# Kernel tuning notes

Measured on AMD Instinct MI355X. Metric: run time of the kernel, lower is better.

## Reference

```python
import jax, jax.numpy as jnp
import numpy as np

N, M, D, C, H = 8192, 8192, 256, 128, 128
LAMBDA_IB = 0.01
EPS = 1e-8


def setup_inputs() -> dict:
    key = jax.random.key(0)
    ks = jax.random.split(key, 8)
    s = 0.05  # small init so exp(critic) stays bounded
    return {
        "x1": jax.random.normal(ks[0], (N, D), jnp.float32),
        "x2": jax.random.normal(ks[1], (M, D), jnp.float32),
        "Wc": (jax.random.normal(ks[2], (D, C), jnp.float32) * s),
        "bc": jnp.zeros((C,), jnp.float32),
        "W1": (jax.random.normal(ks[3], (2 * C, H), jnp.float32) * s),
        "b1": jnp.zeros((H,), jnp.float32),
        "W2": (jax.random.normal(ks[4], (H, H), jnp.float32) * s),
        "b2": jnp.zeros((H,), jnp.float32),
        "W3": (jax.random.normal(ks[5], (H, 1), jnp.float32) * s),
        "b3": jnp.zeros((1,), jnp.float32),
        "perm": jax.random.permutation(ks[6], M).astype(jnp.int32),
    }


def _critic(z, W1, b1, W2, b2, W3, b3):
    h = jax.nn.relu(z @ W1 + b1)
    h = jax.nn.relu(h @ W2 + b2)
    return h @ W3 + b3  # [n, 1]


def reference(x1, x2, Wc, bc, W1, b1, W2, b2, W3, b3, perm):
    # pairwise cosine distance via normalize + GEMM (no NxMxD intermediate)
    n1 = jnp.maximum(jnp.linalg.norm(x1, axis=-1, keepdims=True), EPS)
    n2 = jnp.maximum(jnp.linalg.norm(x2, axis=-1, keepdims=True), EPS)
    distances = 1.0 - (x1 / n1) @ (x2 / n2).T  # [N, M]

    # compressor (shared linear) -> MINE MI lower bound
    xc1 = x1 @ Wc + bc  # [N, C]
    xc2 = x2 @ Wc + bc  # [M, C]
    xy = jnp.concatenate([xc1, xc2], axis=-1)          # joint
    xy_s = jnp.concatenate([xc1, xc2[perm]], axis=-1)  # marginal (shuffled)
    t_xy = _critic(xy, W1, b1, W2, b2, W3, b3)
    t_sh = _critic(xy_s, W1, b1, W2, b2, W3, b3)
    mi = jnp.mean(t_xy) - (jnp.mean(jnp.exp(t_sh)) + jnp.log(jnp.float32(2.0)))
    return distances + LAMBDA_IB * mi
```

## Files before the change

kernel.cpp:

```cpp
#include <hip/hip_runtime.h>
#include <hip/hip_bf16.h>
#include <stdint.h>
#include <stddef.h>


typedef __attribute__((ext_vector_type(8))) short bf16x8;
typedef __attribute__((ext_vector_type(4))) float f32x4;

__device__ __forceinline__ float bf2f(unsigned short u) {
  union { unsigned int i; float f; } a; a.i = ((unsigned int)u) << 16; return a.f;
}
__device__ __forceinline__ unsigned short f2bf(float f) {
  union { float f; unsigned int i; } a; a.f = f;
  unsigned int r = a.i + 0x7fffu + ((a.i >> 16) & 1u);
  return (unsigned short)(r >> 16);
}

#define NROWS 8192
#define DDIM 256
#define CDIM 128
#define HDIM 128

__global__ __launch_bounds__(256) void k_prep_weights(
    const float* __restrict__ Wc, const float* __restrict__ bc,
    const float* __restrict__ W1, const float* __restrict__ b1,
    const float* __restrict__ W2, const float* __restrict__ b2,
    const float* __restrict__ W3, const float* __restrict__ b3,
    unsigned short* __restrict__ WcT, unsigned short* __restrict__ W1T,
    unsigned short* __restrict__ W2T, float* __restrict__ fsmall,
    float* __restrict__ accum) {
  int t = blockIdx.x * 256 + threadIdx.x;
  int T = gridDim.x * 256;
  for (int i = t; i < DDIM * CDIM; i += T) {
    int k = i >> 7, n = i & 127;
    WcT[n * DDIM + k] = f2bf(Wc[i]);
    W1T[n * DDIM + k] = f2bf(W1[i]);
  }
  for (int i = t; i < HDIM * HDIM; i += T) {
    int k = i >> 7, n = i & 127;
    W2T[n * HDIM + k] = f2bf(W2[i]);
  }
  if (blockIdx.x == 0) {
    int tt = threadIdx.x;
    if (tt < 128) {
      fsmall[tt]       = bc[tt];
      fsmall[128 + tt] = b1[tt];
      fsmall[256 + tt] = b2[tt];
      fsmall[384 + tt] = W3[tt];
    }
    if (tt == 0) {
      fsmall[512] = b3[0];
      accum[0] = 0.0f; accum[1] = 0.0f;
    }
  }
}

__global__ __launch_bounds__(256) void k_prep_rows(
    const float* __restrict__ x1, const float* __restrict__ x2,
    unsigned short* __restrict__ xall,
    float* __restrict__ inva, float* __restrict__ invb) {
  int gtid = blockIdx.x * 256 + threadIdx.x;
  int wv = gtid >> 6;
  int lane = threadIdx.x & 63;
  int first = (wv < NROWS);
  const float* src = first ? x1 : x2;
  float* invp = first ? inva : invb;
  int row = first ? wv : wv - NROWS;
  float4 v = *((const float4*)(src + (size_t)row * DDIM) + lane);
  ushort4 o;
  o.x = f2bf(v.x); o.y = f2bf(v.y); o.z = f2bf(v.z); o.w = f2bf(v.w);
  *((ushort4*)(xall + (size_t)wv * DDIM) + lane) = o;
  float ss = v.x * v.x + v.y * v.y + v.z * v.z + v.w * v.w;
#pragma unroll
  for (int off = 32; off > 0; off >>= 1) ss += __shfl_xor(ss, off, 64);
  if (lane == 0) invp[row] = 1.0f / fmaxf(sqrtf(ss), 1e-8f);
}

__global__ __launch_bounds__(256) void k_compress(
    const unsigned short* __restrict__ xall,
    const unsigned short* __restrict__ WcT,
    const float* __restrict__ fsmall,
    unsigned short* __restrict__ xc) {
  int lane = threadIdx.x & 63, wave = threadIdx.x >> 6;
  int lm = lane & 15, lq = lane >> 4;
  int r0 = blockIdx.x * 128 + wave * 32;

  f32x4 acc[2][8];
#pragma unroll
  for (int a = 0; a < 2; ++a)
#pragma unroll
    for (int b = 0; b < 8; ++b) acc[a][b] = (f32x4)(0.0f);

  for (int ks = 0; ks < 8; ++ks) {
    int k = ks * 32 + lq * 8;
    bf16x8 a[2], b[8];
#pragma unroll
    for (int tm = 0; tm < 2; ++tm)
      a[tm] = *(const bf16x8*)(xall + (size_t)(r0 + tm * 16 + lm) * DDIM + k);
#pragma unroll
    for (int nt = 0; nt < 8; ++nt)
      b[nt] = *(const bf16x8*)(WcT + (size_t)(nt * 16 + lm) * DDIM + k);
#pragma unroll
    for (int tm = 0; tm < 2; ++tm)
#pragma unroll
      for (int nt = 0; nt < 8; ++nt)
        acc[tm][nt] = __builtin_amdgcn_mfma_f32_16x16x32_bf16(a[tm], b[nt], acc[tm][nt], 0, 0, 0);
  }

#pragma unroll
  for (int tm = 0; tm < 2; ++tm) {
    int row = r0 + tm * 16 + lq * 4;
#pragma unroll
    for (int nt = 0; nt < 8; ++nt) {
      int col = nt * 16 + lm;
      float bcv = fsmall[col];
#pragma unroll
      for (int r = 0; r < 4; ++r)
        xc[(size_t)(row + r) * CDIM + col] = f2bf(acc[tm][nt][r] + bcv);
    }
  }
}

__global__ __launch_bounds__(256) void k_critic(
    const unsigned short* __restrict__ xc, const int* __restrict__ perm,
    const unsigned short* __restrict__ W1T, const unsigned short* __restrict__ W2T,
    const float* __restrict__ fsmall, float* __restrict__ accum) {
  __shared__ __attribute__((aligned(16))) unsigned short h1buf[4][32][136];
  const float* b1 = fsmall + 128;
  const float* b2 = fsmall + 256;
  const float* W3 = fsmall + 384;
  int lane = threadIdx.x & 63, wave = threadIdx.x >> 6;
  int lm = lane & 15, lq = lane >> 4;
  int v0 = blockIdx.x * 128 + wave * 32;
  bool shuffled = (v0 >= NROWS);

  f32x4 acc[2][8];
#pragma unroll
  for (int a = 0; a < 2; ++a)
#pragma unroll
    for (int b = 0; b < 8; ++b) acc[a][b] = (f32x4)(0.0f);

  for (int ks = 0; ks < 8; ++ks) {
    int k = ks * 32 + lq * 8;
    bf16x8 a[2], b[8];
#pragma unroll
    for (int tm = 0; tm < 2; ++tm) {
      int i = (v0 + tm * 16 + lm) & (NROWS - 1);
      const unsigned short* zp;
      if (k < CDIM) {
        zp = xc + (size_t)i * CDIM + k;
      } else {
        int j = shuffled ? perm[i] : i;
        zp = xc + (size_t)(NROWS + j) * CDIM + (k - CDIM);
      }
      a[tm] = *(const bf16x8*)zp;
    }
#pragma unroll
    for (int nt = 0; nt < 8; ++nt)
      b[nt] = *(const bf16x8*)(W1T + (size_t)(nt * 16 + lm) * DDIM + k);
#pragma unroll
    for (int tm = 0; tm < 2; ++tm)
#pragma unroll
      for (int nt = 0; nt < 8; ++nt)
        acc[tm][nt] = __builtin_amdgcn_mfma_f32_16x16x32_bf16(a[tm], b[nt], acc[tm][nt], 0, 0, 0);
  }

#pragma unroll
  for (int tm = 0; tm < 2; ++tm)
#pragma unroll
    for (int nt = 0; nt < 8; ++nt) {
      int col = nt * 16 + lm;
      float bv = b1[col];
#pragma unroll
      for (int r = 0; r < 4; ++r) {
        int row = tm * 16 + lq * 4 + r;
        h1buf[wave][row][col] = f2bf(fmaxf(acc[tm][nt][r] + bv, 0.0f));
      }
    }
  __syncthreads();

  f32x4 acc2[2][8];
#pragma unroll
  for (int a = 0; a < 2; ++a)
#pragma unroll
    for (int b = 0; b < 8; ++b) acc2[a][b] = (f32x4)(0.0f);
  for (int ks = 0; ks < 4; ++ks) {
    int k = ks * 32 + lq * 8;
    bf16x8 a[2], b[8];
#pragma unroll
    for (int tm = 0; tm < 2; ++tm)
      a[tm] = *(const bf16x8*)&h1buf[wave][tm * 16 + lm][k];
#pragma unroll
    for (int nt = 0; nt < 8; ++nt)
      b[nt] = *(const bf16x8*)(W2T + (size_t)(nt * 16 + lm) * HDIM + k);
#pragma unroll
    for (int tm = 0; tm < 2; ++tm)
#pragma unroll
      for (int nt = 0; nt < 8; ++nt)
        acc2[tm][nt] = __builtin_amdgcn_mfma_f32_16x16x32_bf16(a[tm], b[nt], acc2[tm][nt], 0, 0, 0);
  }

  float part[2][4];
#pragma unroll
  for (int tm = 0; tm < 2; ++tm)
#pragma unroll
    for (int r = 0; r < 4; ++r) part[tm][r] = 0.0f;
#pragma unroll
  for (int nt = 0; nt < 8; ++nt) {
    int col = nt * 16 + lm;
    float w3v = W3[col];
    float b2v = b2[col];
#pragma unroll
    for (int tm = 0; tm < 2; ++tm)
#pragma unroll
      for (int r = 0; r < 4; ++r)
        part[tm][r] += fmaxf(acc2[tm][nt][r] + b2v, 0.0f) * w3v;
  }
#pragma unroll
  for (int m = 1; m <= 8; m <<= 1)
#pragma unroll
    for (int tm = 0; tm < 2; ++tm)
#pragma unroll
      for (int r = 0; r < 4; ++r)
        part[tm][r] += __shfl_xor(part[tm][r], m, 64);

  if (lm == 0) {
    float b3v = fsmall[512];
    float local = 0.0f;
#pragma unroll
    for (int tm = 0; tm < 2; ++tm)
#pragma unroll
      for (int r = 0; r < 4; ++r) {
        float tval = part[tm][r] + b3v;
        local += shuffled ? expf(tval) : tval;
      }
    atomicAdd(&accum[shuffled ? 1 : 0], local);
  }
}

__global__ void k_finalize(const float* __restrict__ accum, float* __restrict__ cadd) {
  float mi = accum[0] / 8192.0f - (accum[1] / 8192.0f + 0.6931471805599453f);
  cadd[0] = 0.01f * mi;
}

#define LDK 72

__global__ __launch_bounds__(256) void k_dist(
    const unsigned short* __restrict__ A,
    const unsigned short* __restrict__ B,
    const float* __restrict__ inva, const float* __restrict__ invb,
    const float* __restrict__ caddp,
    float* __restrict__ out) {
  __shared__ __attribute__((aligned(16))) unsigned short As[128 * LDK];
  __shared__ __attribute__((aligned(16))) unsigned short Bs[128 * LDK];
  int t = threadIdx.x;
  int lane = t & 63, wave = t >> 6;
  int lm = lane & 15, lq = lane >> 4;

  int bid = blockIdx.x;
  int rem = bid & 511;
  int bm = (bid >> 9) * 8 + (rem & 7);
  int bn = rem >> 3;
  int wm = wave >> 1, wn = wave & 1;

  f32x4 acc[4][4];
#pragma unroll
  for (int a = 0; a < 4; ++a)
#pragma unroll
    for (int b = 0; b < 4; ++b) acc[a][b] = (f32x4)(0.0f);

  int srow = t >> 3;
  int sc = (t & 7) * 8;
  const unsigned short* gA = A + (size_t)(bm * 128 + srow) * DDIM + sc;
  const unsigned short* gB = B + (size_t)(bn * 128 + srow) * DDIM + sc;

  for (int kk = 0; kk < 4; ++kk) {
    int k0 = kk * 64;
    bf16x8 va[4], vb[4];
#pragma unroll
    for (int j = 0; j < 4; ++j) {
      va[j] = *(const bf16x8*)(gA + k0 + j * 32 * DDIM);
      vb[j] = *(const bf16x8*)(gB + k0 + j * 32 * DDIM);
    }
    __syncthreads();
#pragma unroll
    for (int j = 0; j < 4; ++j) {
      *(bf16x8*)(As + (srow + j * 32) * LDK + sc) = va[j];
      *(bf16x8*)(Bs + (srow + j * 32) * LDK + sc) = vb[j];
    }
    __syncthreads();
#pragma unroll
    for (int ko = 0; ko < 64; ko += 32) {
      bf16x8 a[4], b[4];
      int cp = ko + lq * 8;
#pragma unroll
      for (int tm = 0; tm < 4; ++tm)
        a[tm] = *(const bf16x8*)(As + (wm * 64 + tm * 16 + lm) * LDK + cp);
#pragma unroll
      for (int tn = 0; tn < 4; ++tn)
        b[tn] = *(const bf16x8*)(Bs + (wn * 64 + tn * 16 + lm) * LDK + cp);
#pragma unroll
      for (int tm = 0; tm < 4; ++tm)
#pragma unroll
        for (int tn = 0; tn < 4; ++tn)
          acc[tm][tn] = __builtin_amdgcn_mfma_f32_16x16x32_bf16(a[tm], b[tn], acc[tm][tn], 0, 0, 0);
    }
  }

  float cadd = *caddp;
#pragma unroll
  for (int tm = 0; tm < 4; ++tm) {
    int gr0 = bm * 128 + wm * 64 + tm * 16 + lq * 4;
#pragma unroll
    for (int tn = 0; tn < 4; ++tn) {
      int gc = bn * 128 + wn * 64 + tn * 16 + lm;
      float ib = invb[gc];
#pragma unroll
      for (int r = 0; r < 4; ++r)
        out[(size_t)(gr0 + r) * 8192 + gc] =
            1.0f - acc[tm][tn][r] * inva[gr0 + r] * ib + cadd;
    }
  }
}

extern "C" void kernel_launch(void* const* d_in, const int* in_sizes, int n_in,
                              void* d_out, int out_size, void* d_ws, size_t ws_size,
                              hipStream_t stream) {
  const float* x1 = (const float*)d_in[0];
  const float* x2 = (const float*)d_in[1];
  const float* Wc = (const float*)d_in[2];
  const float* bc = (const float*)d_in[3];
  const float* W1 = (const float*)d_in[4];
  const float* b1 = (const float*)d_in[5];
  const float* W2 = (const float*)d_in[6];
  const float* b2 = (const float*)d_in[7];
  const float* W3 = (const float*)d_in[8];
  const float* b3 = (const float*)d_in[9];
  const int* perm = (const int*)d_in[10];
  float* out = (float*)d_out;

  char* ws = (char*)d_ws;
  unsigned short* xall = (unsigned short*)ws;
  unsigned short* xc   = (unsigned short*)(ws + (8u << 20));
  unsigned short* WcT  = (unsigned short*)(ws + (12u << 20));
  unsigned short* W1T  = (unsigned short*)(ws + (12u << 20) + 65536);
  unsigned short* W2T  = (unsigned short*)(ws + (12u << 20) + 131072);
  float* fsmall = (float*)(ws + (12u << 20) + 163840);
  float* inva  = (float*)(ws + (12u << 20) + 167936);
  float* invb  = (float*)(ws + (12u << 20) + 200704);
  float* accum = (float*)(ws + (12u << 20) + 233472);
  float* cadd  = (float*)(ws + (12u << 20) + 233480);

  k_prep_weights<<<32, 256, 0, stream>>>(Wc, bc, W1, b1, W2, b2, W3, b3,
                                         WcT, W1T, W2T, fsmall, accum);
  k_prep_rows<<<4096, 256, 0, stream>>>(x1, x2, xall, inva, invb);
  k_compress<<<128, 256, 0, stream>>>(xall, WcT, fsmall, xc);
  k_critic<<<128, 256, 0, stream>>>(xc, perm, W1T, W2T, fsmall, accum);
  k_finalize<<<1, 1, 0, stream>>>(accum, cadd);
  k_dist<<<4096, 256, 0, stream>>>(xall, xall + (size_t)NROWS * DDIM,
                                   inva, invb, cadd, out);
}
```

Measured before the change: 394.0 us.

## Merge prep kernels, fold finalize into dist, use direct global-to-LDS loads

Merges the weight-prep and row-prep kernels into one launch and drops the finalize kernel, so the MI constant is computed inside the distance kernel's epilogue. The compress and critic kernels now give each wave 16 rows and launch 256 blocks, doubling parallelism on the small GEMMs. The distance GEMM stages tiles with global_load_lds straight into unpadded shared memory instead of going through registers. Dropping the LDS padding can cause bank conflicts on the MFMA operand reads, and the single-buffered direct loads still wait on vmcnt(0) before every compute step.

```diff
diff --git a/kernel.cpp b/kernel.cpp
--- a/kernel.cpp
+++ b/kernel.cpp
@@ -16,49 +16,28 @@
   return (unsigned short)(r >> 16);
 }
 
+__device__ __forceinline__ void gl16(const unsigned short* g, unsigned short* l) {
+  __builtin_amdgcn_global_load_lds(
+      (const __attribute__((address_space(1))) void*)g,
+      (__attribute__((address_space(3))) void*)l, 16, 0, 0);
+}
+
 #define NROWS 8192
 #define DDIM 256
 #define CDIM 128
 #define HDIM 128
 
-__global__ __launch_bounds__(256) void k_prep_weights(
+__global__ __launch_bounds__(256) void k_prep(
+    const float* __restrict__ x1, const float* __restrict__ x2,
     const float* __restrict__ Wc, const float* __restrict__ bc,
     const float* __restrict__ W1, const float* __restrict__ b1,
     const float* __restrict__ W2, const float* __restrict__ b2,
     const float* __restrict__ W3, const float* __restrict__ b3,
+    unsigned short* __restrict__ xall,
+    float* __restrict__ inva, float* __restrict__ invb,
     unsigned short* __restrict__ WcT, unsigned short* __restrict__ W1T,
     unsigned short* __restrict__ W2T, float* __restrict__ fsmall,
     float* __restrict__ accum) {
-  int t = blockIdx.x * 256 + threadIdx.x;
-  int T = gridDim.x * 256;
-  for (int i = t; i < DDIM * CDIM; i += T) {
-    int k = i >> 7, n = i & 127;
-    WcT[n * DDIM + k] = f2bf(Wc[i]);
-    W1T[n * DDIM + k] = f2bf(W1[i]);
-  }
-  for (int i = t; i < HDIM * HDIM; i += T) {
-    int k = i >> 7, n = i & 127;
-    W2T[n * HDIM + k] = f2bf(W2[i]);
-  }
-  if (blockIdx.x == 0) {
-    int tt = threadIdx.x;
-    if (tt < 128) {
-      fsmall[tt]       = bc[tt];
-      fsmall[128 + tt] = b1[tt];
-      fsmall[256 + tt] = b2[tt];
-      fsmall[384 + tt] = W3[tt];
-    }
-    if (tt == 0) {
-      fsmall[512] = b3[0];
-      accum[0] = 0.0f; accum[1] = 0.0f;
-    }
-  }
-}
-
-__global__ __launch_bounds__(256) void k_prep_rows(
-    const float* __restrict__ x1, const float* __restrict__ x2,
-    unsigned short* __restrict__ xall,
-    float* __restrict__ inva, float* __restrict__ invb) {
   int gtid = blockIdx.x * 256 + threadIdx.x;
   int wv = gtid >> 6;
   int lane = threadIdx.x & 63;
@@ -74,6 +53,33 @@
 #pragma unroll
   for (int off = 32; off > 0; off >>= 1) ss += __shfl_xor(ss, off, 64);
   if (lane == 0) invp[row] = 1.0f / fmaxf(sqrtf(ss), 1e-8f);
+
+  if (blockIdx.x < 32) {
+    int t = blockIdx.x * 256 + threadIdx.x;
+    const int T = 32 * 256;
+    for (int i = t; i < DDIM * CDIM; i += T) {
+      int k = i >> 7, n = i & 127;
+      WcT[n * DDIM + k] = f2bf(Wc[i]);
+      W1T[n * DDIM + k] = f2bf(W1[i]);
+    }
+    for (int i = t; i < HDIM * HDIM; i += T) {
+      int k = i >> 7, n = i & 127;
+      W2T[n * HDIM + k] = f2bf(W2[i]);
+    }
+    if (blockIdx.x == 0) {
+      int tt = threadIdx.x;
+      if (tt < 128) {
+        fsmall[tt]       = bc[tt];
+        fsmall[128 + tt] = b1[tt];
+        fsmall[256 + tt] = b2[tt];
+        fsmall[384 + tt] = W3[tt];
+      }
+      if (tt == 0) {
+        fsmall[512] = b3[0];
+        accum[0] = 0.0f; accum[1] = 0.0f;
+      }
+    }
+  }
 }
 
 __global__ __launch_bounds__(256) void k_compress(
@@ -83,41 +89,32 @@
     unsigned short* __restrict__ xc) {
   int lane = threadIdx.x & 63, wave = threadIdx.x >> 6;
   int lm = lane & 15, lq = lane >> 4;
-  int r0 = blockIdx.x * 128 + wave * 32;
-
-  f32x4 acc[2][8];
-#pragma unroll
-  for (int a = 0; a < 2; ++a)
-#pragma unroll
-    for (int b = 0; b < 8; ++b) acc[a][b] = (f32x4)(0.0f);
+  int r0 = blockIdx.x * 64 + wave * 16;
+
+  f32x4 acc[8];
+#pragma unroll
+  for (int b = 0; b < 8; ++b) acc[b] = (f32x4)(0.0f);
 
   for (int ks = 0; ks < 8; ++ks) {
     int k = ks * 32 + lq * 8;
-    bf16x8 a[2], b[8];
-#pragma unroll
-    for (int tm = 0; tm < 2; ++tm)
-      a[tm] = *(const bf16x8*)(xall + (size_t)(r0 + tm * 16 + lm) * DDIM + k);
+    bf16x8 a = *(const bf16x8*)(xall + (size_t)(r0 + lm) * DDIM + k);
+    bf16x8 b[8];
 #pragma unroll
     for (int nt = 0; nt < 8; ++nt)
       b[nt] = *(const bf16x8*)(WcT + (size_t)(nt * 16 + lm) * DDIM + k);
 #pragma unroll
-    for (int tm = 0; tm < 2; ++tm)
-#pragma unroll
-      for (int nt = 0; nt < 8; ++nt)
-        acc[tm][nt] = __builtin_amdgcn_mfma_f32_16x16x32_bf16(a[tm], b[nt], acc[tm][nt], 0, 0, 0);
-  }
-
-#pragma unroll
-  for (int tm = 0; tm < 2; ++tm) {
-    int row = r0 + tm * 16 + lq * 4;
-#pragma unroll
-    for (int nt = 0; nt < 8; ++nt) {
-      int col = nt * 16 + lm;
-      float bcv = fsmall[col];
-#pragma unroll
-      for (int r = 0; r < 4; ++r)
-        xc[(size_t)(row + r) * CDIM + col] = f2bf(acc[tm][nt][r] + bcv);
-    }
+    for (int nt = 0; nt < 8; ++nt)
+      acc[nt] = __builtin_amdgcn_mfma_f32_16x16x32_bf16(a, b[nt], acc[nt], 0, 0, 0);
+  }
+
+  int row = r0 + lq * 4;
+#pragma unroll
+  for (int nt = 0; nt < 8; ++nt) {
+    int col = nt * 16 + lm;
+    float bcv = fsmall[col];
+#pragma unroll
+    for (int r = 0; r < 4; ++r)
+      xc[(size_t)(row + r) * CDIM + col] = f2bf(acc[nt][r] + bcv);
   }
 }
 
@@ -125,134 +122,100 @@
     const unsigned short* __restrict__ xc, const int* __restrict__ perm,
     const unsigned short* __restrict__ W1T, const unsigned short* __restrict__ W2T,
     const float* __restrict__ fsmall, float* __restrict__ accum) {
-  __shared__ __attribute__((aligned(16))) unsigned short h1buf[4][32][136];
+  __shared__ __attribute__((aligned(16))) unsigned short h1buf[4][16][136];
   const float* b1 = fsmall + 128;
   const float* b2 = fsmall + 256;
   const float* W3 = fsmall + 384;
   int lane = threadIdx.x & 63, wave = threadIdx.x >> 6;
   int lm = lane & 15, lq = lane >> 4;
-  int v0 = blockIdx.x * 128 + wave * 32;
-  bool shuffled = (v0 >= NROWS);
-
-  f32x4 acc[2][8];
-#pragma unroll
-  for (int a = 0; a < 2; ++a)
-#pragma unroll
-    for (int b = 0; b < 8; ++b) acc[a][b] = (f32x4)(0.0f);
+  int v0 = blockIdx.x * 64 + wave * 16;
+  bool shuffled = (blockIdx.x * 64 >= NROWS);
+
+  f32x4 acc[8];
+#pragma unroll
+  for (int b = 0; b < 8; ++b) acc[b] = (f32x4)(0.0f);
 
   for (int ks = 0; ks < 8; ++ks) {
     int k = ks * 32 + lq * 8;
-    bf16x8 a[2], b[8];
-#pragma unroll
-    for (int tm = 0; tm < 2; ++tm) {
-      int i = (v0 + tm * 16 + lm) & (NROWS - 1);
-      const unsigned short* zp;
-      if (k < CDIM) {
-        zp = xc + (size_t)i * CDIM + k;
-      } else {
-        int j = shuffled ? perm[i] : i;
-        zp = xc + (size_t)(NROWS + j) * CDIM + (k - CDIM);
-      }
-      a[tm] = *(const bf16x8*)zp;
-    }
+    int i = (v0 + lm) & (NROWS - 1);
+    const unsigned short* zp;
+    if (k < CDIM) {
+      zp = xc + (size_t)i * CDIM + k;
+    } else {
+      int j = shuffled ? perm[i] : i;
+      zp = xc + (size_t)(NROWS + j) * CDIM + (k - CDIM);
+    }
+    bf16x8 a = *(const bf16x8*)zp;
+    bf16x8 b[8];
 #pragma unroll
     for (int nt = 0; nt < 8; ++nt)
       b[nt] = *(const bf16x8*)(W1T + (size_t)(nt * 16 + lm) * DDIM + k);
 #pragma unroll
-    for (int tm = 0; tm < 2; ++tm)
-#pragma unroll
-      for (int nt = 0; nt < 8; ++nt)
-        acc[tm][nt] = __builtin_amdgcn_mfma_f32_16x16x32_bf16(a[tm], b[nt], acc[tm][nt], 0, 0, 0);
-  }
-
-#pragma unroll
-  for (int tm = 0; tm < 2; ++tm)
-#pragma unroll
-    for (int nt = 0; nt < 8; ++nt) {
-      int col = nt * 16 + lm;
-      float bv = b1[col];
-#pragma unroll
-      for (int r = 0; r < 4; ++r) {
-        int row = tm * 16 + lq * 4 + r;
-        h1buf[wave][row][col] = f2bf(fmaxf(acc[tm][nt][r] + bv, 0.0f));
-      }
-    }
+    for (int nt = 0; nt < 8; ++nt)
+      acc[nt] = __builtin_amdgcn_mfma_f32_16x16x32_bf16(a, b[nt], acc[nt], 0, 0, 0);
+  }
+
+#pragma unroll
+  for (int nt = 0; nt < 8; ++nt) {
+    int col = nt * 16 + lm;
+    float bv = b1[col];
+#pragma unroll
+    for (int r = 0; r < 4; ++r)
+      h1buf[wave][lq * 4 + r][col] = f2bf(fmaxf(acc[nt][r] + bv, 0.0f));
+  }
   __syncthreads();
 
-  f32x4 acc2[2][8];
-#pragma unroll
-  for (int a = 0; a < 2; ++a)
-#pragma unroll
-    for (int b = 0; b < 8; ++b) acc2[a][b] = (f32x4)(0.0f);
+  f32x4 acc2[8];
+#pragma unroll
+  for (int b = 0; b < 8; ++b) acc2[b] = (f32x4)(0.0f);
   for (int ks = 0; ks < 4; ++ks) {
     int k = ks * 32 + lq * 8;
-    bf16x8 a[2], b[8];
-#pragma unroll
-    for (int tm = 0; tm < 2; ++tm)
-      a[tm] = *(const bf16x8*)&h1buf[wave][tm * 16 + lm][k];
+    bf16x8 a = *(const bf16x8*)&h1buf[wave][lm][k];
+    bf16x8 b[8];
 #pragma unroll
     for (int nt = 0; nt < 8; ++nt)
       b[nt] = *(const bf16x8*)(W2T + (size_t)(nt * 16 + lm) * HDIM + k);
 #pragma unroll
-    for (int tm = 0; tm < 2; ++tm)
-#pragma unroll
-      for (int nt = 0; nt < 8; ++nt)
-        acc2[tm][nt] = __builtin_amdgcn_mfma_f32_16x16x32_bf16(a[tm], b[nt], acc2[tm][nt], 0, 0, 0);
-  }
-
-  float part[2][4];
-#pragma unroll
-  for (int tm = 0; tm < 2; ++tm)
-#pragma unroll
-    for (int r = 0; r < 4; ++r) part[tm][r] = 0.0f;
+    for (int nt = 0; nt < 8; ++nt)
+      acc2[nt] = __builtin_amdgcn_mfma_f32_16x16x32_bf16(a, b[nt], acc2[nt], 0, 0, 0);
+  }
+
+  float part[4] = {0.0f, 0.0f, 0.0f, 0.0f};
 #pragma unroll
   for (int nt = 0; nt < 8; ++nt) {
     int col = nt * 16 + lm;
     float w3v = W3[col];
     float b2v = b2[col];
 #pragma unroll
-    for (int tm = 0; tm < 2; ++tm)
-#pragma unroll
-      for (int r = 0; r < 4; ++r)
-        part[tm][r] += fmaxf(acc2[tm][nt][r] + b2v, 0.0f) * w3v;
+    for (int r = 0; r < 4; ++r)
+      part[r] += fmaxf(acc2[nt][r] + b2v, 0.0f) * w3v;
   }
 #pragma unroll
   for (int m = 1; m <= 8; m <<= 1)
 #pragma unroll
-    for (int tm = 0; tm < 2; ++tm)
-#pragma unroll
-      for (int r = 0; r < 4; ++r)
-        part[tm][r] += __shfl_xor(part[tm][r], m, 64);
+    for (int r = 0; r < 4; ++r)
+      part[r] += __shfl_xor(part[r], m, 64);
 
   if (lm == 0) {
     float b3v = fsmall[512];
     float local = 0.0f;
 #pragma unroll
-    for (int tm = 0; tm < 2; ++tm)
-#pragma unroll
-      for (int r = 0; r < 4; ++r) {
-        float tval = part[tm][r] + b3v;
-        local += shuffled ? expf(tval) : tval;
-      }
+    for (int r = 0; r < 4; ++r) {
+      float tval = part[r] + b3v;
+      local += shuffled ? expf(tval) : tval;
+    }
     atomicAdd(&accum[shuffled ? 1 : 0], local);
   }
 }
-
-__global__ void k_finalize(const float* __restrict__ accum, float* __restrict__ cadd) {
-  float mi = accum[0] / 8192.0f - (accum[1] / 8192.0f + 0.6931471805599453f);
-  cadd[0] = 0.01f * mi;
-}
-
-#define LDK 72
 
 __global__ __launch_bounds__(256) void k_dist(
     const unsigned short* __restrict__ A,
     const unsigned short* __restrict__ B,
     const float* __restrict__ inva, const float* __restrict__ invb,
-    const float* __restrict__ caddp,
+    const float* __restrict__ accum,
     float* __restrict__ out) {
-  __shared__ __attribute__((aligned(16))) unsigned short As[128 * LDK];
-  __shared__ __attribute__((aligned(16))) unsigned short Bs[128 * LDK];
+  __shared__ __attribute__((aligned(16))) unsigned short As[128 * 64];
+  __shared__ __attribute__((aligned(16))) unsigned short Bs[128 * 64];
   int t = threadIdx.x;
   int lane = t & 63, wave = t >> 6;
   int lm = lane & 15, lq = lane >> 4;
@@ -273,21 +236,18 @@
   int sc = (t & 7) * 8;
   const unsigned short* gA = A + (size_t)(bm * 128 + srow) * DDIM + sc;
   const unsigned short* gB = B + (size_t)(bn * 128 + srow) * DDIM + sc;
+  unsigned short* lA = As + srow * 64 + sc;
+  unsigned short* lB = Bs + srow * 64 + sc;
 
   for (int kk = 0; kk < 4; ++kk) {
     int k0 = kk * 64;
-    bf16x8 va[4], vb[4];
+    __syncthreads();
 #pragma unroll
     for (int j = 0; j < 4; ++j) {
-      va[j] = *(const bf16x8*)(gA + k0 + j * 32 * DDIM);
-      vb[j] = *(const bf16x8*)(gB + k0 + j * 32 * DDIM);
-    }
-    __syncthreads();
-#pragma unroll
-    for (int j = 0; j < 4; ++j) {
-      *(bf16x8*)(As + (srow + j * 32) * LDK + sc) = va[j];
-      *(bf16x8*)(Bs + (srow + j * 32) * LDK + sc) = vb[j];
-    }
+      gl16(gA + k0 + j * 32 * DDIM, lA + j * 32 * 64);
+      gl16(gB + k0 + j * 32 * DDIM, lB + j * 32 * 64);
+    }
+    asm volatile("s_waitcnt vmcnt(0)" ::: "memory");
     __syncthreads();
 #pragma unroll
     for (int ko = 0; ko < 64; ko += 32) {
@@ -295,10 +255,10 @@
       int cp = ko + lq * 8;
 #pragma unroll
       for (int tm = 0; tm < 4; ++tm)
-        a[tm] = *(const bf16x8*)(As + (wm * 64 + tm * 16 + lm) * LDK + cp);
+        a[tm] = *(const bf16x8*)(As + (wm * 64 + tm * 16 + lm) * 64 + cp);
 #pragma unroll
       for (int tn = 0; tn < 4; ++tn)
-        b[tn] = *(const bf16x8*)(Bs + (wn * 64 + tn * 16 + lm) * LDK + cp);
+        b[tn] = *(const bf16x8*)(Bs + (wn * 64 + tn * 16 + lm) * 64 + cp);
 #pragma unroll
       for (int tm = 0; tm < 4; ++tm)
 #pragma unroll
@@ -307,7 +267,8 @@
     }
   }
 
-  float cadd = *caddp;
+  float cadd = 0.01f * ((accum[0] - accum[1]) * (1.0f / 8192.0f)
+                        - 0.6931471805599453f);
 #pragma unroll
   for (int tm = 0; tm < 4; ++tm) {
     int gr0 = bm * 128 + wm * 64 + tm * 16 + lq * 4;
@@ -349,14 +310,11 @@
   float* inva  = (float*)(ws + (12u << 20) + 167936);
   float* invb  = (float*)(ws + (12u << 20) + 200704);
   float* accum = (float*)(ws + (12u << 20) + 233472);
-  float* cadd  = (float*)(ws + (12u << 20) + 233480);
-
-  k_prep_weights<<<32, 256, 0, stream>>>(Wc, bc, W1, b1, W2, b2, W3, b3,
-                                         WcT, W1T, W2T, fsmall, accum);
-  k_prep_rows<<<4096, 256, 0, stream>>>(x1, x2, xall, inva, invb);
-  k_compress<<<128, 256, 0, stream>>>(xall, WcT, fsmall, xc);
-  k_critic<<<128, 256, 0, stream>>>(xc, perm, W1T, W2T, fsmall, accum);
-  k_finalize<<<1, 1, 0, stream>>>(accum, cadd);
+
+  k_prep<<<4096, 256, 0, stream>>>(x1, x2, Wc, bc, W1, b1, W2, b2, W3, b3,
+                                   xall, inva, invb, WcT, W1T, W2T, fsmall, accum);
+  k_compress<<<256, 256, 0, stream>>>(xall, WcT, fsmall, xc);
+  k_critic<<<256, 256, 0, stream>>>(xc, perm, W1T, W2T, fsmall, accum);
   k_dist<<<4096, 256, 0, stream>>>(xall, xall + (size_t)NROWS * DDIM,
-                                   inva, invb, cadd, out);
-}
+                                   inva, invb, accum, out);
+}
```

Result: faster. 379.6 us (-3.6%).
